# Kernel tuning notes

Measured on AMD Instinct MI355X. Metric: run time of the kernel, lower is better.

## Reference

```python
import jax, jax.numpy as jnp
import numpy as np

B, N, F_IN, F_OUT = 8, 8192, 64, 64
LN_EPS = 1e-5


def setup_inputs() -> dict:
    key = jax.random.key(0)
    k_x, k_adj, k_ws, k_wn = jax.random.split(key, 4)
    scale = 1.0 / np.sqrt(F_IN)
    return {
        "x": jax.random.normal(k_x, (B, N, F_IN), dtype=jnp.float32),
        "adj_matrix": jax.random.randint(k_adj, (N, N), 0, 2, dtype=jnp.int32),
        "W_self": jax.random.normal(k_ws, (F_IN, F_OUT), dtype=jnp.float32) * scale,
        "b_self": jnp.zeros((F_OUT,), dtype=jnp.float32),
        "W_neigh": jax.random.normal(k_wn, (F_IN, F_OUT), dtype=jnp.float32) * scale,
        "b_neigh": jnp.zeros((F_OUT,), dtype=jnp.float32),
        "ln_gamma": jnp.ones((F_OUT,), dtype=jnp.float32),
        "ln_beta": jnp.zeros((F_OUT,), dtype=jnp.float32),
    }


def reference(x, adj_matrix, W_self, b_self, W_neigh, b_neigh, ln_gamma, ln_beta):
    # GraphSAGE 'mean' conv (vectorized form of the per-node python loop):
    # agg[b,i,:] = mean over neighbors j (adj[i,j] > 0) of x[b,j,:]
    A = (adj_matrix > 0).astype(x.dtype)                 # [N, N]
    deg = A.sum(axis=1)                                  # [N]
    agg = jnp.einsum('ij,bjf->bif', A, x)                # [B, N, F_in]
    agg = agg / jnp.maximum(deg, 1.0)[None, :, None]
    neigh_out = agg @ W_neigh + b_neigh                  # [B, N, F_out]
    # nodes with no neighbors keep zeros (loop never writes them)
    neigh_out = jnp.where((deg > 0)[None, :, None], neigh_out, 0.0)
    self_out = x @ W_self + b_self                       # [B, N, F_out]
    out = jax.nn.relu(self_out + neigh_out)              # SAGE internal relu
    # GCNBlock: relu (idempotent here) -> LayerNorm; dropout is eval-mode identity
    out = jax.nn.relu(out)
    mu = out.mean(axis=-1, keepdims=True)
    var = jnp.mean((out - mu) ** 2, axis=-1, keepdims=True)
    out = (out - mu) * jax.lax.rsqrt(var + LN_EPS) * ln_gamma + ln_beta
    return out
```

## Files before the change

### kernel.cpp

```cpp
#include <hip/hip_runtime.h>

#define NN 8192

typedef __bf16 bf16x8 __attribute__((ext_vector_type(8)));
typedef float f32x4 __attribute__((ext_vector_type(4)));
typedef unsigned short u16x8 __attribute__((ext_vector_type(8)));
typedef int i32x4 __attribute__((ext_vector_type(4)));
typedef int i32x16 __attribute__((ext_vector_type(16)));

#define GLOBAL_AS __attribute__((address_space(1)))
#define LDS_AS __attribute__((address_space(3)))

__device__ __forceinline__ unsigned short f2bf(float f) {
  unsigned int u = __builtin_bit_cast(unsigned int, f);
  u += 0x7FFFu + ((u >> 16) & 1u);
  return (unsigned short)(u >> 16);
}
__device__ __forceinline__ float bf2f(unsigned short b) {
  unsigned int u = ((unsigned int)b) << 16;
  return __builtin_bit_cast(float, u);
}

__device__ __forceinline__ i32x4 expA(unsigned int h) {
  i32x4 a;
  a[0] = (int)((((h      ) & 0xFu) * 0x204081u) & 0x01010101u);
  a[1] = (int)((((h >> 4 ) & 0xFu) * 0x204081u) & 0x01010101u);
  a[2] = (int)((((h >> 8 ) & 0xFu) * 0x204081u) & 0x01010101u);
  a[3] = (int)((((h >> 12) & 0xFu) * 0x204081u) & 0x01010101u);
  return a;
}

__global__ __launch_bounds__(256) void pack_kernel(
    const int* __restrict__ adj, unsigned long long* __restrict__ maskT,
    float* __restrict__ degp) {
  __shared__ __align__(16) unsigned char xb[4][1024];
  const int lane = threadIdx.x & 63;
  const int wv = threadIdx.x >> 6;
  const int bid = blockIdx.x;
  const int row = ((bid & 7) << 10) + ((bid >> 3) << 1) + (wv >> 1);
  const int half = wv & 1;
  const int* src = adj + (size_t)row * NN + half * 4096;
  unsigned int nib[16];
#pragma unroll
  for (int c = 0; c < 16; ++c) {
    int4 v = *(const int4*)(src + c * 256 + lane * 4);
    nib[c] = (unsigned int)(v.x > 0)
           | ((unsigned int)(v.y > 0) << 1)
           | ((unsigned int)(v.z > 0) << 2)
           | ((unsigned int)(v.w > 0) << 3);
  }
#pragma unroll
  for (int c = 0; c < 16; ++c) xb[wv][c * 64 + lane] = (unsigned char)nib[c];
  __syncthreads();
  uint4 B = *(const uint4*)&xb[wv][lane * 16];
  unsigned int t0 = (B.x | (B.x >> 4)) & 0x00FF00FFu; t0 = (t0 | (t0 >> 8)) & 0xFFFFu;
  unsigned int t1 = (B.y | (B.y >> 4)) & 0x00FF00FFu; t1 = (t1 | (t1 >> 8)) & 0xFFFFu;
  unsigned int t2 = (B.z | (B.z >> 4)) & 0x00FF00FFu; t2 = (t2 | (t2 >> 8)) & 0xFFFFu;
  unsigned int t3 = (B.w | (B.w >> 4)) & 0x00FF00FFu; t3 = (t3 | (t3 >> 8)) & 0xFFFFu;
  unsigned long long word = (unsigned long long)(t0 | (t1 << 16))
                          | ((unsigned long long)(t2 | (t3 << 16)) << 32);
  const size_t P = (size_t)((half << 5) + (lane >> 1));
  maskT[(P * NN + row) * 2 + (lane & 1)] = word;
  int deg = (int)__popcll(word);
#pragma unroll
  for (int m = 1; m < 64; m <<= 1) deg += __shfl_xor(deg, m);
  if (lane == 0) degp[half * NN + row] = (float)deg;
}

__global__ __launch_bounds__(256) void prep_kernel(
    const float* __restrict__ x, const float* __restrict__ Wself,
    const float* __restrict__ bself, const float* __restrict__ Wneigh,
    char* __restrict__ Yq, unsigned short* __restrict__ Sout) {
  __shared__ __align__(16) unsigned short xa[64 * 64];
  __shared__ __align__(16) unsigned short bm[128 * 64];
  const int t = threadIdx.x;
  const int b = blockIdx.x >> 7;
  const int j0 = (blockIdx.x & 127) << 6;

  {
    const float* Wsel = (t < 128) ? Wneigh : Wself;
    const int tt = t & 127;
    const int k = tt >> 1;
    const int c0 = (tt & 1) << 5;
    const int nbase = (t < 128) ? 0 : 64;
    const float4* src = (const float4*)(Wsel + k * 64 + c0);
#pragma unroll
    for (int q = 0; q < 8; ++q) {
      float4 v = src[q];
      int n0 = nbase + c0 + q * 4;
      int n;
      n = n0 + 0; bm[n * 64 + (k ^ ((n & 7) << 3))] = f2bf(v.x);
      n = n0 + 1; bm[n * 64 + (k ^ ((n & 7) << 3))] = f2bf(v.y);
      n = n0 + 2; bm[n * 64 + (k ^ ((n & 7) << 3))] = f2bf(v.z);
      n = n0 + 3; bm[n * 64 + (k ^ ((n & 7) << 3))] = f2bf(v.w);
    }
  }
  {
    const int j = t >> 2, q = t & 3;
    const float* xrow = x + ((size_t)b * NN + j0 + j) * 64 + q * 16;
    float4 v0 = *(const float4*)(xrow + 0);
    float4 v1 = *(const float4*)(xrow + 4);
    float4 v2 = *(const float4*)(xrow + 8);
    float4 v3 = *(const float4*)(xrow + 12);
    u16x8 p0, p1;
    p0[0] = f2bf(v0.x); p0[1] = f2bf(v0.y); p0[2] = f2bf(v0.z); p0[3] = f2bf(v0.w);
    p0[4] = f2bf(v1.x); p0[5] = f2bf(v1.y); p0[6] = f2bf(v1.z); p0[7] = f2bf(v1.w);
    p1[0] = f2bf(v2.x); p1[1] = f2bf(v2.y); p1[2] = f2bf(v2.z); p1[3] = f2bf(v2.w);
    p1[4] = f2bf(v3.x); p1[5] = f2bf(v3.y); p1[6] = f2bf(v3.z); p1[7] = f2bf(v3.w);
    const int base = q * 16;
    const int sw = (j & 7) << 3;
    *(u16x8*)&xa[j * 64 + (base ^ sw)] = p0;
    *(u16x8*)&xa[j * 64 + ((base + 8) ^ sw)] = p1;
  }
  __syncthreads();

  const int lane = t & 63, w = t >> 6;
  const int rl = lane & 15, hi = lane >> 4;
  f32x4 acc[8];
#pragma unroll
  for (int i = 0; i < 8; ++i) acc[i] = (f32x4){0.f, 0.f, 0.f, 0.f};

#pragma unroll
  for (int ks = 0; ks < 2; ++ks) {
    const int r = w * 16 + rl;
    const int kel = ks * 32 + hi * 8;
    bf16x8 af = __builtin_bit_cast(bf16x8, *(u16x8*)&xa[r * 64 + (kel ^ ((r & 7) << 3))]);
#pragma unroll
    for (int nf = 0; nf < 8; ++nf) {
      const int n = nf * 16 + rl;
      bf16x8 bv = __builtin_bit_cast(bf16x8, *(u16x8*)&bm[n * 64 + (kel ^ ((n & 7) << 3))]);
      acc[nf] = __builtin_amdgcn_mfma_f32_16x16x32_bf16(af, bv, acc[nf], 0, 0, 0);
    }
  }
#pragma unroll
  for (int nf = 0; nf < 8; ++nf) {
    if (nf < 4) {
      const int n = nf * 16 + rl;
      unsigned int pkt = 0;
#pragma unroll
      for (int r = 0; r < 4; ++r) {
        float v = fminf(fmaxf(acc[nf][r] * 16.0f, -127.0f), 127.0f);
        int iv = __float2int_rn(v);
        pkt |= ((unsigned int)(iv & 0xFF)) << (r * 8);
      }
      *(unsigned int*)(Yq + (size_t)(b * 64 + n) * NN + j0 + w * 16 + hi * 4) = pkt;
    } else {
      const int fo = (nf - 4) * 16 + rl;
      const float bsv = bself[fo];
#pragma unroll
      for (int r = 0; r < 4; ++r) {
        const int jj = w * 16 + hi * 4 + r;
        Sout[((size_t)b * NN + j0 + jj) * 64 + fo] = f2bf(acc[nf][r] + bsv);
      }
    }
  }
}

__global__ __launch_bounds__(512, 1) void gemm_kernel(
    const i32x4* __restrict__ mask,
    const char* __restrict__ Yq,
    unsigned short* __restrict__ Cp) {
  __shared__ __align__(16) char yL[8][8192];
  const int tid = threadIdx.x;
  const int lane = tid & 63, w = tid >> 6;
  const int nid = ((blockIdx.x & 7) << 5) + (blockIdx.x >> 3);
  const int q = nid >> 4, mb = nid & 15;
  const int ksp = q >> 3, nb = q & 7;
  const int i0 = mb << 9;
  const int kbase = ksp << 12;
  const int ncol0 = nb << 6;
  const int l31 = lane & 31, l5 = lane >> 5;
  const int hs16 = l5 << 4;

  const int cst = (w << 3) + (lane >> 3);
  const char* ysrc = Yq + (size_t)(ncol0 + cst) * NN + kbase
                     + (((lane & 7) ^ (cst & 7)) << 4);
  const i32x4* mqT = mask + ((size_t)(ksp << 5)) * NN + i0 + (w << 6) + l31;

  int boff[2][4];
#pragma unroll
  for (int nf = 0; nf < 2; ++nf)
#pragma unroll
    for (int s = 0; s < 4; ++s) {
      const int col = (nf << 5) + l31;
      const int g = (s << 1) + l5;
      boff[nf][s] = (col << 7) + ((g ^ (col & 7)) << 4);
    }

  i32x16 acc[2][2];
#pragma unroll
  for (int mf = 0; mf < 2; ++mf)
#pragma unroll
    for (int nf = 0; nf < 2; ++nf)
#pragma unroll
      for (int e = 0; e < 16; ++e) acc[mf][nf][e] = 0;

#define BARRIER  __builtin_amdgcn_s_barrier()
#define MEMBAR   asm volatile("" ::: "memory")
#define WAIT_VM4 asm volatile("s_waitcnt vmcnt(4)" ::: "memory")

#define STAGE(t)                                                              \
  __builtin_amdgcn_global_load_lds(                                           \
      (GLOBAL_AS void*)const_cast<char*>(ysrc + (size_t)((t) & 31) * 128),    \
      (LDS_AS void*)&yL[(t) & 7][w << 10], 16, 0, 0)

#define LOADM(M0, M1, t)                                                      \
  { M0 = mqT[(size_t)((t) & 31) * NN]; M1 = mqT[(size_t)((t) & 31) * NN + 32]; }

#define COMPUTE(t, M0, M1)                                                    \
  {                                                                           \
    const char* yb_ = &yL[(t) & 7][0];                                        \
    __builtin_amdgcn_s_setprio(1);                                            \
    _Pragma("unroll")                                                         \
    for (int s_ = 0; s_ < 4; ++s_) {                                          \
      i32x4 b0_ = *(const i32x4*)(yb_ + boff[0][s_]);                         \
      i32x4 b1_ = *(const i32x4*)(yb_ + boff[1][s_]);                         \
      unsigned int h0_ = (unsigned int)(M0)[s_] >> hs16;                      \
      unsigned int h1_ = (unsigned int)(M1)[s_] >> hs16;                      \
      i32x4 a0_ = expA(h0_);                                                  \
      i32x4 a1_ = expA(h1_);                                                  \
      acc[0][0] = __builtin_amdgcn_mfma_i32_32x32x32_i8(a0_, b0_, acc[0][0], 0, 0, 0); \
      acc[0][1] = __builtin_amdgcn_mfma_i32_32x32x32_i8(a0_, b1_, acc[0][1], 0, 0, 0); \
      acc[1][0] = __builtin_amdgcn_mfma_i32_32x32x32_i8(a1_, b0_, acc[1][0], 0, 0, 0); \
      acc[1][1] = __builtin_amdgcn_mfma_i32_32x32x32_i8(a1_, b1_, acc[1][1], 0, 0, 0); \
    }                                                                         \
    __builtin_amdgcn_s_setprio(0);                                            \
  }

  i32x4 Ma0, Ma1, Mb0, Mb1;
  STAGE(0);
  STAGE(1);
  LOADM(Ma0, Ma1, 0);
  STAGE(2);

  for (int t2 = 0; t2 < 32; t2 += 2) {
    LOADM(Mb0, Mb1, t2 + 1);
    STAGE(t2 + 3);
    WAIT_VM4;
    BARRIER; MEMBAR;
    COMPUTE(t2, Ma0, Ma1);
    LOADM(Ma0, Ma1, t2 + 2);
    STAGE(t2 + 4);
    WAIT_VM4;
    BARRIER; MEMBAR;
    COMPUTE(t2 + 1, Mb0, Mb1);
  }
  asm volatile("s_waitcnt vmcnt(0)" ::: "memory");

#pragma unroll
  for (int mf = 0; mf < 2; ++mf)
#pragma unroll
    for (int nf = 0; nf < 2; ++nf) {
      const int col = ncol0 + (nf << 5) + l31;
#pragma unroll
      for (int r = 0; r < 16; ++r) {
        const int row = i0 + (w << 6) + (mf << 5) + (r & 3) + ((r >> 2) << 3) + (l5 << 2);
        Cp[((size_t)ksp * NN + row) * 512 + col] = f2bf((float)acc[mf][nf][r] * 0.0625f);
      }
    }
#undef BARRIER
#undef MEMBAR
#undef WAIT_VM4
#undef STAGE
#undef LOADM
#undef COMPUTE
}

__global__ __launch_bounds__(256) void epi_kernel(
    const unsigned short* __restrict__ Cp, const float* __restrict__ degp,
    const unsigned short* __restrict__ Sbf, const float* __restrict__ bneigh,
    const float* __restrict__ gamma, const float* __restrict__ beta,
    float* __restrict__ out) {
  const int lane = threadIdx.x & 63;
  const int wid = (blockIdx.x << 2) + (threadIdx.x >> 6);
  const int b = wid >> 13;
  const int i = wid & (NN - 1);
  const float deg = degp[i] + degp[NN + i];
  const float rdeg = 1.0f / fmaxf(deg, 1.0f);
  const size_t cidx = (size_t)i * 512 + b * 64 + lane;
  const float c = bf2f(Cp[cidx]) + bf2f(Cp[(size_t)NN * 512 + cidx]);
  const float sv = bf2f(Sbf[((size_t)b * NN + i) * 64 + lane]);
  float v = sv + ((deg > 0.5f) ? (c * rdeg + bneigh[lane]) : 0.0f);
  v = fmaxf(v, 0.0f);
  float s1 = v, s2 = v * v;
#pragma unroll
  for (int m = 1; m < 64; m <<= 1) {
    s1 += __shfl_xor(s1, m);
    s2 += __shfl_xor(s2, m);
  }
  const float mu = s1 * 0.015625f;
  const float var = s2 * 0.015625f - mu * mu;
  const float o = (v - mu) * rsqrtf(var + 1e-5f) * gamma[lane] + beta[lane];
  out[((size_t)b * NN + i) * 64 + lane] = o;
}

extern "C" void kernel_launch(void* const* d_in, const int* in_sizes, int n_in,
                              void* d_out, int out_size, void* d_ws, size_t ws_size,
                              hipStream_t stream) {
  (void)in_sizes; (void)n_in; (void)out_size; (void)ws_size;
  const float* x      = (const float*)d_in[0];
  const int*   adj    = (const int*)d_in[1];
  const float* Wself  = (const float*)d_in[2];
  const float* bself  = (const float*)d_in[3];
  const float* Wneigh = (const float*)d_in[4];
  const float* bneigh = (const float*)d_in[5];
  const float* gamma  = (const float*)d_in[6];
  const float* beta   = (const float*)d_in[7];
  char* ws = (char*)d_ws;
  char*               Yq    = ws;
  unsigned long long* maskT = (unsigned long long*)(ws + 4194304);
  unsigned short*     Sbf   = (unsigned short*)(ws + 12582912);
  unsigned short*     Cp    = (unsigned short*)(ws + 20971520);
  float*              degp  = (float*)(ws + 37748736);
  float*              out   = (float*)d_out;

  pack_kernel<<<dim3(4096), dim3(256), 0, stream>>>(adj, maskT, degp);
  prep_kernel<<<dim3(1024), dim3(256), 0, stream>>>(x, Wself, bself, Wneigh, Yq, Sbf);
  gemm_kernel<<<dim3(256), dim3(512), 0, stream>>>((const i32x4*)maskT, Yq, Cp);
  epi_kernel<<<dim3(16384), dim3(256), 0, stream>>>(Cp, degp, Sbf, bneigh, gamma, beta, out);
}
```

Before: 119.1 us.

## Merge pack and prep kernels; retile GEMM to 256-thread blocks, two per CU

Result: no change. 118.9 us (-0.1%).

```diff
diff --git a/kernel.cpp b/kernel.cpp
--- a/kernel.cpp
+++ b/kernel.cpp
@@ -30,52 +30,55 @@
   return a;
 }
 
-__global__ __launch_bounds__(256) void pack_kernel(
+__global__ __launch_bounds__(256) void packprep_kernel(
     const int* __restrict__ adj, unsigned long long* __restrict__ maskT,
-    float* __restrict__ degp) {
-  __shared__ __align__(16) unsigned char xb[4][1024];
-  const int lane = threadIdx.x & 63;
-  const int wv = threadIdx.x >> 6;
-  const int bid = blockIdx.x;
-  const int row = ((bid & 7) << 10) + ((bid >> 3) << 1) + (wv >> 1);
-  const int half = wv & 1;
-  const int* src = adj + (size_t)row * NN + half * 4096;
-  unsigned int nib[16];
-#pragma unroll
-  for (int c = 0; c < 16; ++c) {
-    int4 v = *(const int4*)(src + c * 256 + lane * 4);
-    nib[c] = (unsigned int)(v.x > 0)
-           | ((unsigned int)(v.y > 0) << 1)
-           | ((unsigned int)(v.z > 0) << 2)
-           | ((unsigned int)(v.w > 0) << 3);
-  }
-#pragma unroll
-  for (int c = 0; c < 16; ++c) xb[wv][c * 64 + lane] = (unsigned char)nib[c];
-  __syncthreads();
-  uint4 B = *(const uint4*)&xb[wv][lane * 16];
-  unsigned int t0 = (B.x | (B.x >> 4)) & 0x00FF00FFu; t0 = (t0 | (t0 >> 8)) & 0xFFFFu;
-  unsigned int t1 = (B.y | (B.y >> 4)) & 0x00FF00FFu; t1 = (t1 | (t1 >> 8)) & 0xFFFFu;
-  unsigned int t2 = (B.z | (B.z >> 4)) & 0x00FF00FFu; t2 = (t2 | (t2 >> 8)) & 0xFFFFu;
-  unsigned int t3 = (B.w | (B.w >> 4)) & 0x00FF00FFu; t3 = (t3 | (t3 >> 8)) & 0xFFFFu;
-  unsigned long long word = (unsigned long long)(t0 | (t1 << 16))
-                          | ((unsigned long long)(t2 | (t3 << 16)) << 32);
-  const size_t P = (size_t)((half << 5) + (lane >> 1));
-  maskT[(P * NN + row) * 2 + (lane & 1)] = word;
-  int deg = (int)__popcll(word);
-#pragma unroll
-  for (int m = 1; m < 64; m <<= 1) deg += __shfl_xor(deg, m);
-  if (lane == 0) degp[half * NN + row] = (float)deg;
-}
-
-__global__ __launch_bounds__(256) void prep_kernel(
+    float* __restrict__ degp,
     const float* __restrict__ x, const float* __restrict__ Wself,
     const float* __restrict__ bself, const float* __restrict__ Wneigh,
     char* __restrict__ Yq, unsigned short* __restrict__ Sout) {
+  __shared__ __align__(16) unsigned char xb[4][1024];
   __shared__ __align__(16) unsigned short xa[64 * 64];
   __shared__ __align__(16) unsigned short bm[128 * 64];
+
+  if (blockIdx.x < 4096) {
+    const int lane = threadIdx.x & 63;
+    const int wv = threadIdx.x >> 6;
+    const int bid = blockIdx.x;
+    const int row = ((bid & 7) << 10) + ((bid >> 3) << 1) + (wv >> 1);
+    const int half = wv & 1;
+    const int* src = adj + (size_t)row * NN + half * 4096;
+    unsigned int nib[16];
+#pragma unroll
+    for (int c = 0; c < 16; ++c) {
+      int4 v = *(const int4*)(src + c * 256 + lane * 4);
+      nib[c] = (unsigned int)(v.x > 0)
+             | ((unsigned int)(v.y > 0) << 1)
+             | ((unsigned int)(v.z > 0) << 2)
+             | ((unsigned int)(v.w > 0) << 3);
+    }
+#pragma unroll
+    for (int c = 0; c < 16; ++c) xb[wv][c * 64 + lane] = (unsigned char)nib[c];
+    __syncthreads();
+    uint4 B = *(const uint4*)&xb[wv][lane * 16];
+    unsigned int t0 = (B.x | (B.x >> 4)) & 0x00FF00FFu; t0 = (t0 | (t0 >> 8)) & 0xFFFFu;
+    unsigned int t1 = (B.y | (B.y >> 4)) & 0x00FF00FFu; t1 = (t1 | (t1 >> 8)) & 0xFFFFu;
+    unsigned int t2 = (B.z | (B.z >> 4)) & 0x00FF00FFu; t2 = (t2 | (t2 >> 8)) & 0xFFFFu;
+    unsigned int t3 = (B.w | (B.w >> 4)) & 0x00FF00FFu; t3 = (t3 | (t3 >> 8)) & 0xFFFFu;
+    unsigned long long word = (unsigned long long)(t0 | (t1 << 16))
+                            | ((unsigned long long)(t2 | (t3 << 16)) << 32);
+    const size_t P = (size_t)((half << 5) + (lane >> 1));
+    maskT[(P * NN + row) * 2 + (lane & 1)] = word;
+    int deg = (int)__popcll(word);
+#pragma unroll
+    for (int m = 1; m < 64; m <<= 1) deg += __shfl_xor(deg, m);
+    if (lane == 0) degp[half * NN + row] = (float)deg;
+    return;
+  }
+
   const int t = threadIdx.x;
-  const int b = blockIdx.x >> 7;
-  const int j0 = (blockIdx.x & 127) << 6;
+  const int pb = blockIdx.x - 4096;
+  const int b = pb >> 7;
+  const int j0 = (pb & 127) << 6;
 
   {
     const float* Wsel = (t < 128) ? Wneigh : Wself;
@@ -156,23 +159,24 @@
   }
 }
 
-__global__ __launch_bounds__(512, 1) void gemm_kernel(
+__global__ __launch_bounds__(256, 2) void gemm_kernel(
     const i32x4* __restrict__ mask,
     const char* __restrict__ Yq,
     unsigned short* __restrict__ Cp) {
   __shared__ __align__(16) char yL[8][8192];
   const int tid = threadIdx.x;
   const int lane = tid & 63, w = tid >> 6;
-  const int nid = ((blockIdx.x & 7) << 5) + (blockIdx.x >> 3);
-  const int q = nid >> 4, mb = nid & 15;
-  const int ksp = q >> 3, nb = q & 7;
-  const int i0 = mb << 9;
+  const int nid = ((blockIdx.x & 7) << 6) + (blockIdx.x >> 3);
+  const int ksp = nid >> 8;
+  const int nb = (nid >> 5) & 7;
+  const int mb = nid & 31;
+  const int i0 = mb << 8;
   const int kbase = ksp << 12;
   const int ncol0 = nb << 6;
   const int l31 = lane & 31, l5 = lane >> 5;
   const int hs16 = l5 << 4;
 
-  const int cst = (w << 3) + (lane >> 3);
+  const int cst = (w << 4) + (lane >> 3);
   const char* ysrc = Yq + (size_t)(ncol0 + cst) * NN + kbase
                      + (((lane & 7) ^ (cst & 7)) << 4);
   const i32x4* mqT = mask + ((size_t)(ksp << 5)) * NN + i0 + (w << 6) + l31;
@@ -197,12 +201,18 @@
 
 #define BARRIER  __builtin_amdgcn_s_barrier()
 #define MEMBAR   asm volatile("" ::: "memory")
-#define WAIT_VM4 asm volatile("s_waitcnt vmcnt(4)" ::: "memory")
+#define WAIT_VM6 asm volatile("s_waitcnt vmcnt(6)" ::: "memory")
 
 #define STAGE(t)                                                              \
-  __builtin_amdgcn_global_load_lds(                                           \
-      (GLOBAL_AS void*)const_cast<char*>(ysrc + (size_t)((t) & 31) * 128),    \
-      (LDS_AS void*)&yL[(t) & 7][w << 10], 16, 0, 0)
+  {                                                                           \
+    __builtin_amdgcn_global_load_lds(                                         \
+        (GLOBAL_AS void*)const_cast<char*>(ysrc + (size_t)((t) & 31) * 128),  \
+        (LDS_AS void*)&yL[(t) & 7][w << 11], 16, 0, 0);                       \
+    __builtin_amdgcn_global_load_lds(                                         \
+        (GLOBAL_AS void*)const_cast<char*>(ysrc + (size_t)8 * NN              \
+                                           + (size_t)((t) & 31) * 128),       \
+        (LDS_AS void*)&yL[(t) & 7][(w << 11) + 1024], 16, 0, 0);              \
+  }
 
 #define LOADM(M0, M1, t)                                                      \
   { M0 = mqT[(size_t)((t) & 31) * NN]; M1 = mqT[(size_t)((t) & 31) * NN + 32]; }
@@ -230,18 +240,18 @@
   i32x4 Ma0, Ma1, Mb0, Mb1;
   STAGE(0);
   STAGE(1);
+  STAGE(2);
   LOADM(Ma0, Ma1, 0);
-  STAGE(2);
 
   for (int t2 = 0; t2 < 32; t2 += 2) {
     LOADM(Mb0, Mb1, t2 + 1);
     STAGE(t2 + 3);
-    WAIT_VM4;
+    WAIT_VM6;
     BARRIER; MEMBAR;
     COMPUTE(t2, Ma0, Ma1);
     LOADM(Ma0, Ma1, t2 + 2);
     STAGE(t2 + 4);
-    WAIT_VM4;
+    WAIT_VM6;
     BARRIER; MEMBAR;
     COMPUTE(t2 + 1, Mb0, Mb1);
   }
@@ -260,7 +270,7 @@
     }
 #undef BARRIER
 #undef MEMBAR
-#undef WAIT_VM4
+#undef WAIT_VM6
 #undef STAGE
 #undef LOADM
 #undef COMPUTE
@@ -314,8 +324,8 @@
   float*              degp  = (float*)(ws + 37748736);
   float*              out   = (float*)d_out;
 
-  pack_kernel<<<dim3(4096), dim3(256), 0, stream>>>(adj, maskT, degp);
-  prep_kernel<<<dim3(1024), dim3(256), 0, stream>>>(x, Wself, bself, Wneigh, Yq, Sbf);
-  gemm_kernel<<<dim3(256), dim3(512), 0, stream>>>((const i32x4*)maskT, Yq, Cp);
+  packprep_kernel<<<dim3(5120), dim3(256), 0, stream>>>(
+      adj, maskT, degp, x, Wself, bself, Wneigh, Yq, Sbf);
+  gemm_kernel<<<dim3(512), dim3(256), 0, stream>>>((const i32x4*)maskT, Yq, Cp);
   epi_kernel<<<dim3(16384), dim3(256), 0, stream>>>(Cp, degp, Sbf, bneigh, gamma, beta, out);
 }
```
